# Performance work log

Measured on AMD Instinct MI355X. Metric: run time of the kernel, lower is better.

## Reference

```python
import jax, jax.numpy as jnp
import numpy as np

# Junction tree: C0=(X0,X1f,X2), C1=(X1c,X2,X3f), C2=(X2,X3c,X4)
D0, D1F, D1C, D2, D3F, D3C, D4 = 256, 1024, 256, 256, 512, 256, 512


def _sel(fine: int, coarse: int) -> jnp.ndarray:
    """0/1 selection matrix [fine, coarse]: M[f, f // (fine//coarse)] = 1.
    Equivalent to torch_to_matrix_mul(arange(fine), arange(fine)//r, fine, coarse)."""
    r = fine // coarse
    return (jnp.arange(fine)[:, None] // r == jnp.arange(coarse)[None, :]).astype(jnp.float32)


def setup_inputs() -> dict:
    key = jax.random.key(0)
    k0, k1, k2 = jax.random.split(key, 3)
    theta0 = jax.random.normal(k0, (D0, D1F, D2), dtype=jnp.float32)
    theta1 = jax.random.normal(k1, (D1C, D2, D3F), dtype=jnp.float32)
    theta2 = jax.random.normal(k2, (D2, D3C, D4), dtype=jnp.float32)
    m_x1_fwd = _sel(D1F, D1C)          # (1024, 256): fine X1 -> coarse X1
    m_x1_bwd = m_x1_fwd.T              # (256, 1024): coarse X1 -> fine X1
    m_x3_fwd = _sel(D3F, D3C)          # (512, 256)
    m_x3_bwd = m_x3_fwd.T              # (256, 512)
    return dict(theta0=theta0, theta1=theta1, theta2=theta2,
                m_x1_fwd=m_x1_fwd, m_x1_bwd=m_x1_bwd,
                m_x3_fwd=m_x3_fwd, m_x3_bwd=m_x3_bwd)


def reference(theta0, theta1, theta2, m_x1_fwd, m_x1_bwd, m_x3_fwd, m_x3_bwd):
    # --- forward message C0 -> C1: sum over X0, map X1 fine->coarse, X2 passthrough
    msg01 = jnp.einsum('jc,jf->fc', theta0.sum(axis=0), m_x1_fwd)   # (D1C, D2)
    theta1 = theta1 + msg01[:, :, None]                             # reshape_dims (T,T,F)
    # --- forward message C1 -> C2: sum over X1, X2 passthrough, map X3 fine->coarse
    msg12 = jnp.einsum('cj,jf->cf', theta1.sum(axis=0), m_x3_fwd)   # (D2, D3C)
    theta2 = theta2 + msg12[:, :, None]
    # --- backward message C2 -> C1: sum over X4, subtract stored fwd msg, map X3 coarse->fine
    msg21 = jnp.einsum('cj,jf->cf', theta2.sum(axis=2) - msg12, m_x3_bwd)  # (D2, D3F)
    theta1 = theta1 + msg21[None, :, :]                             # reshape_dims (F,T,T)
    # --- backward message C1 -> C0: sum over X3, subtract stored fwd msg, map X1 coarse->fine
    msg10 = jnp.einsum('jc,jf->fc', theta1.sum(axis=2) - msg01, m_x1_bwd)  # (D1F, D2)
    theta0 = theta0 + msg10[None, :, :]
    return (theta0, theta1, theta2)
```

## Files before the change

### kernel.cpp

```cpp
#include <hip/hip_runtime.h>

#define D0   256
#define D1F  1024
#define D1C  256
#define D2   256
#define D3F  512
#define D3C  256
#define D4   512

#define CB   64
#define NCB  4

#define OFF_MSG01 0
#define OFF_S10   65536
#define OFF_S12   196608
#define OFF_S22   262144
#define OFF_MSG12 327680
#define OFF_S3    393216

typedef float f4 __attribute__((ext_vector_type(4)));

__device__ __forceinline__ float wave_sum(float s) {
#pragma unroll
  for (int off = 32; off; off >>= 1) s += __shfl_down(s, off);
  return s;
}
__device__ __forceinline__ float wave_allsum(float s) {
#pragma unroll
  for (int off = 32; off; off >>= 1) s += __shfl_xor(s, off);
  return s;
}

__global__ __launch_bounds__(256) void k_stage1(const float* __restrict__ t0,
                                                const float* __restrict__ t1,
                                                float* __restrict__ ws, int cb) {
  const int t = threadIdx.x, lane = t & 63, w = t >> 6;
  __shared__ f4 lds[4][2][64];
  if (blockIdx.x < 1024) {
    const int bx = blockIdx.x;
    const int c  = cb * CB + (bx & 63);
    const int ac = bx >> 6;
    float* S10 = ws + OFF_S10;
    float* S12 = ws + OFF_S12;
    f4 accA = {0.f, 0.f, 0.f, 0.f};
    f4 accB = {0.f, 0.f, 0.f, 0.f};
#pragma unroll
    for (int ii = 0; ii < 4; ++ii) {
      const int a = ac * 16 + ii * 4 + w;
      const f4* row = (const f4*)(t1 + ((size_t)a * D2 + c) * D3F);
      f4 v0 = row[lane];
      f4 v1 = row[lane + 64];
      accA += v0; accB += v1;
      float s = v0.x + v0.y + v0.z + v0.w + v1.x + v1.y + v1.z + v1.w;
      s = wave_sum(s);
      if (lane == 0) S12[a * D2 + c] = s;
    }
    lds[w][0][lane] = accA;
    lds[w][1][lane] = accB;
    __syncthreads();
    if (t < 128) {
      const int which = t >> 6, l = t & 63;
      f4 s = lds[0][which][l] + lds[1][which][l] + lds[2][which][l] + lds[3][which][l];
      float* dst = &S10[(size_t)c * D3F + which * 256 + 4 * l];
      atomicAdd(dst + 0, s.x);
      atomicAdd(dst + 1, s.y);
      atomicAdd(dst + 2, s.z);
      atomicAdd(dst + 3, s.w);
    }
  } else {
    const int bx = blockIdx.x - 1024;
    const int f = bx & 255, ic = bx >> 8;
    float* msg01 = ws + OFF_MSG01;
    const int c4 = lane & 15, jr = lane >> 4;
    const int j = 4 * f + jr;
    const f4* t0v = (const f4*)t0;
    f4 acc = {0.f, 0.f, 0.f, 0.f};
#pragma unroll
    for (int ii = 0; ii < 4; ++ii) {
      const int i = ic * 16 + w * 4 + ii;
      acc += t0v[((size_t)i * D1F + j) * 64 + cb * 16 + c4];
    }
#pragma unroll
    for (int off = 32; off >= 16; off >>= 1) {
      acc.x += __shfl_down(acc.x, off);
      acc.y += __shfl_down(acc.y, off);
      acc.z += __shfl_down(acc.z, off);
      acc.w += __shfl_down(acc.w, off);
    }
    if (jr == 0) lds[w][0][c4] = acc;
    __syncthreads();
    if (t < 16) {
      f4 s = lds[0][0][t] + lds[1][0][t] + lds[2][0][t] + lds[3][0][t];
      float* dst = &msg01[f * D2 + cb * CB + 4 * t];
      atomicAdd(dst + 0, s.x);
      atomicAdd(dst + 1, s.y);
      atomicAdd(dst + 2, s.z);
      atomicAdd(dst + 3, s.w);
    }
  }
}

__global__ __launch_bounds__(256) void k_w2mm(const float* __restrict__ t2,
                                              float* __restrict__ out2,
                                              float* __restrict__ ws, int cb) {
  const float* msg01 = ws + OFF_MSG01;
  const float* S10   = ws + OFF_S10;
  float* msg12 = ws + OFF_MSG12;
  float* S22   = ws + OFF_S22;
  const int bx = blockIdx.x;
  const int c = cb * CB + (bx & 63), fc = bx >> 6;
  const int t = threadIdx.x, lane = t & 63, w = t >> 6;
  float p = msg01[lane * D2 + c] + msg01[(lane + 64) * D2 + c]
          + msg01[(lane + 128) * D2 + c] + msg01[(lane + 192) * D2 + c];
  p = wave_allsum(p);
  const float* S10c = S10 + (size_t)c * D3F;
#pragma unroll
  for (int ii = 0; ii < 4; ++ii) {
    const int f = fc * 16 + ii * 4 + w;
    const float m = S10c[2 * f] + S10c[2 * f + 1] + 2.f * p;
    if (lane == 0) msg12[c * D3C + f] = m;
    const size_t base4 = ((size_t)c * D3C + f) * (D4 / 4);
    const f4* row = (const f4*)t2 + base4;
    f4* orow = (f4*)out2 + base4;
    f4 v0 = __builtin_nontemporal_load(row + lane);
    f4 v1 = __builtin_nontemporal_load(row + lane + 64);
    __builtin_nontemporal_store(v0 + m, orow + lane);
    __builtin_nontemporal_store(v1 + m, orow + lane + 64);
    float s = v0.x + v0.y + v0.z + v0.w + v1.x + v1.y + v1.z + v1.w;
    s = wave_sum(s);
    if (lane == 0) S22[c * D3C + f] = s;
  }
}

__global__ __launch_bounds__(256) void k_w1s3(const float* __restrict__ t1,
                                              float* __restrict__ out1,
                                              float* __restrict__ ws, int cb) {
  const float* msg01 = ws + OFF_MSG01;
  const float* S22   = ws + OFF_S22;
  const float* msg12 = ws + OFF_MSG12;
  const int t = threadIdx.x;
  __shared__ float red[4];
  if (blockIdx.x < 8192) {
    const size_t idx = (size_t)blockIdx.x * 256 + t;
    const int k4 = (int)(idx & 127);
    const int cl = (int)((idx >> 7) & 63);
    const int a  = (int)(idx >> 13);
    const int c  = cb * CB + cl;
    const size_t addr = ((size_t)a * D2 + c) * (D3F / 4) + k4;
    f4 v = ((const f4*)t1)[addr];
    const float m = msg01[a * D2 + c];
    const float2 s22v = ((const float2*)S22)[c * 128 + k4];
    const float2 m12v = ((const float2*)msg12)[c * 128 + k4];
    const float s2a = m + s22v.x + 511.f * m12v.x;
    const float s2b = m + s22v.y + 511.f * m12v.y;
    f4 o;
    o.x = v.x + s2a; o.y = v.y + s2a; o.z = v.z + s2b; o.w = v.w + s2b;
    __builtin_nontemporal_store(o, (f4*)out1 + addr);
  } else {
    const float* S12 = ws + OFF_S12;
    float* s3 = ws + OFF_S3;
    const int c = cb * CB + (int)(blockIdx.x - 8192);
    const int lane = t & 63, w = t >> 6;
    const float s2v = S22[c * D3C + t] + 511.f * msg12[c * D3C + t];
    float p = wave_sum(s2v);
    if (lane == 0) red[w] = p;
    __syncthreads();
    const float rs = red[0] + red[1] + red[2] + red[3];
    s3[t * D2 + c] = S12[t * D2 + c] + 511.f * msg01[t * D2 + c] + 2.f * rs;
  }
}

__global__ __launch_bounds__(256) void k_w0(const float* __restrict__ t0,
                                            float* __restrict__ out0,
                                            const float* __restrict__ ws, int cb) {
  const f4* s3v = (const f4*)(ws + OFF_S3);
  const size_t idx = (size_t)blockIdx.x * 256 + threadIdx.x;
  const int c4 = (int)(idx & 15);
  const int j  = (int)((idx >> 4) & 1023);
  const int i  = (int)(idx >> 14);
  const size_t addr = ((size_t)i * D1F + j) * 64 + cb * 16 + c4;
  f4 v = ((const f4*)t0)[addr];
  f4 m = s3v[(j >> 2) * 64 + cb * 16 + c4];
  __builtin_nontemporal_store(v + m, (f4*)out0 + addr);
}

extern "C" void kernel_launch(void* const* d_in, const int* in_sizes, int n_in,
                              void* d_out, int out_size, void* d_ws, size_t ws_size,
                              hipStream_t stream) {
  const float* t0 = (const float*)d_in[0];
  const float* t1 = (const float*)d_in[1];
  const float* t2 = (const float*)d_in[2];
  float* out0 = (float*)d_out;
  float* out1 = out0 + (size_t)D0 * D1F * D2;
  float* out2 = out1 + (size_t)D1C * D2 * D3F;
  float* ws = (float*)d_ws;

  hipMemsetAsync(d_ws, 0, (size_t)OFF_S12 * sizeof(float), stream);

  for (int cb = 0; cb < NCB; ++cb) {
    k_stage1<<<5120, 256, 0, stream>>>(t0, t1, ws, cb);
    k_w2mm<<<1024, 256, 0, stream>>>(t2, out2, ws, cb);
    k_w1s3<<<8256, 256, 0, stream>>>(t1, out1, ws, cb);
    k_w0<<<16384, 256, 0, stream>>>(t0, out0, ws, cb);
  }
}
```

Measured before the change: 958.0 us.

## Drop column chunking and fuse update kernels into single full-width passes

Removes the four-way split over the X2 column dimension, so each stage runs once over the full tensors. The two reductions, the t2 update and a new small s2/s3 kernel each run once. A single merged kernel then writes both the theta1 and theta0 outputs with fully contiguous indexing. The theta0 reduction now reads whole 1KB rows per wave instead of 256B segments and no longer needs the cross-lane shuffle. This cuts launch count from sixteen to four and improves access contiguity. In exchange it gives up the per-chunk working set (about 96MB of t0 and t1) that could stay resident in the last-level cache between the reduce pass and the update pass.

```diff
diff --git a/kernel.cpp b/kernel.cpp
--- a/kernel.cpp
+++ b/kernel.cpp
@@ -8,15 +8,13 @@
 #define D3C  256
 #define D4   512
 
-#define CB   64
-#define NCB  4
-
 #define OFF_MSG01 0
 #define OFF_S10   65536
 #define OFF_S12   196608
 #define OFF_S22   262144
 #define OFF_MSG12 327680
-#define OFF_S3    393216
+#define OFF_S2    393216
+#define OFF_S3    458752
 
 typedef float f4 __attribute__((ext_vector_type(4)));
 
@@ -31,15 +29,15 @@
   return s;
 }
 
-__global__ __launch_bounds__(256) void k_stage1(const float* __restrict__ t0,
+__global__ __launch_bounds__(256) void k_reduce(const float* __restrict__ t0,
                                                 const float* __restrict__ t1,
-                                                float* __restrict__ ws, int cb) {
+                                                float* __restrict__ ws) {
   const int t = threadIdx.x, lane = t & 63, w = t >> 6;
-  __shared__ f4 lds[4][2][64];
-  if (blockIdx.x < 1024) {
+  __shared__ f4 lds[512];
+  if (blockIdx.x < 4096) {
     const int bx = blockIdx.x;
-    const int c  = cb * CB + (bx & 63);
-    const int ac = bx >> 6;
+    const int c  = bx & 255;
+    const int ac = bx >> 8;
     float* S10 = ws + OFF_S10;
     float* S12 = ws + OFF_S12;
     f4 accA = {0.f, 0.f, 0.f, 0.f};
@@ -55,12 +53,13 @@
       s = wave_sum(s);
       if (lane == 0) S12[a * D2 + c] = s;
     }
-    lds[w][0][lane] = accA;
-    lds[w][1][lane] = accB;
+    lds[w * 128 + lane]      = accA;
+    lds[w * 128 + 64 + lane] = accB;
     __syncthreads();
     if (t < 128) {
       const int which = t >> 6, l = t & 63;
-      f4 s = lds[0][which][l] + lds[1][which][l] + lds[2][which][l] + lds[3][which][l];
+      f4 s = lds[which * 64 + l] + lds[128 + which * 64 + l]
+           + lds[256 + which * 64 + l] + lds[384 + which * 64 + l];
       float* dst = &S10[(size_t)c * D3F + which * 256 + 4 * l];
       atomicAdd(dst + 0, s.x);
       atomicAdd(dst + 1, s.y);
@@ -68,30 +67,23 @@
       atomicAdd(dst + 3, s.w);
     }
   } else {
-    const int bx = blockIdx.x - 1024;
+    const int bx = blockIdx.x - 4096;
     const int f = bx & 255, ic = bx >> 8;
     float* msg01 = ws + OFF_MSG01;
-    const int c4 = lane & 15, jr = lane >> 4;
-    const int j = 4 * f + jr;
+    const int c4 = lane;
+    const int j = 4 * f + w;
     const f4* t0v = (const f4*)t0;
     f4 acc = {0.f, 0.f, 0.f, 0.f};
 #pragma unroll
-    for (int ii = 0; ii < 4; ++ii) {
-      const int i = ic * 16 + w * 4 + ii;
-      acc += t0v[((size_t)i * D1F + j) * 64 + cb * 16 + c4];
+    for (int it = 0; it < 16; ++it) {
+      const int i = ic * 16 + it;
+      acc += t0v[((size_t)i * D1F + j) * 64 + c4];
     }
-#pragma unroll
-    for (int off = 32; off >= 16; off >>= 1) {
-      acc.x += __shfl_down(acc.x, off);
-      acc.y += __shfl_down(acc.y, off);
-      acc.z += __shfl_down(acc.z, off);
-      acc.w += __shfl_down(acc.w, off);
-    }
-    if (jr == 0) lds[w][0][c4] = acc;
+    lds[t] = acc;
     __syncthreads();
-    if (t < 16) {
-      f4 s = lds[0][0][t] + lds[1][0][t] + lds[2][0][t] + lds[3][0][t];
-      float* dst = &msg01[f * D2 + cb * CB + 4 * t];
+    if (t < 64) {
+      f4 s = lds[t] + lds[t + 64] + lds[t + 128] + lds[t + 192];
+      float* dst = &msg01[f * D2 + 4 * t];
       atomicAdd(dst + 0, s.x);
       atomicAdd(dst + 1, s.y);
       atomicAdd(dst + 2, s.z);
@@ -102,13 +94,13 @@
 
 __global__ __launch_bounds__(256) void k_w2mm(const float* __restrict__ t2,
                                               float* __restrict__ out2,
-                                              float* __restrict__ ws, int cb) {
+                                              float* __restrict__ ws) {
   const float* msg01 = ws + OFF_MSG01;
   const float* S10   = ws + OFF_S10;
   float* msg12 = ws + OFF_MSG12;
   float* S22   = ws + OFF_S22;
   const int bx = blockIdx.x;
-  const int c = cb * CB + (bx & 63), fc = bx >> 6;
+  const int c = bx & 255, fc = bx >> 8;
   const int t = threadIdx.x, lane = t & 63, w = t >> 6;
   float p = msg01[lane * D2 + c] + msg01[(lane + 64) * D2 + c]
           + msg01[(lane + 128) * D2 + c] + msg01[(lane + 192) * D2 + c];
@@ -132,56 +124,54 @@
   }
 }
 
-__global__ __launch_bounds__(256) void k_w1s3(const float* __restrict__ t1,
-                                              float* __restrict__ out1,
-                                              float* __restrict__ ws, int cb) {
+__global__ __launch_bounds__(256) void k_s2s3(float* __restrict__ ws) {
   const float* msg01 = ws + OFF_MSG01;
+  const float* S12   = ws + OFF_S12;
   const float* S22   = ws + OFF_S22;
   const float* msg12 = ws + OFF_MSG12;
+  float* s2          = ws + OFF_S2;
+  float* s3          = ws + OFF_S3;
+  const int c = blockIdx.x, t = threadIdx.x;
+  const float s2v = S22[c * D3C + t] + 511.f * msg12[c * D3C + t];
+  s2[c * D3C + t] = s2v;
+  float p = wave_sum(s2v);
+  __shared__ float red[4];
+  if ((t & 63) == 0) red[t >> 6] = p;
+  __syncthreads();
+  const float rs = red[0] + red[1] + red[2] + red[3];
+  s3[t * D2 + c] = S12[t * D2 + c] + 511.f * msg01[t * D2 + c] + 2.f * rs;
+}
+
+__global__ __launch_bounds__(256) void k_w1w0(const float* __restrict__ t0,
+                                              const float* __restrict__ t1,
+                                              float* __restrict__ out0,
+                                              float* __restrict__ out1,
+                                              const float* __restrict__ ws) {
   const int t = threadIdx.x;
-  __shared__ float red[4];
-  if (blockIdx.x < 8192) {
+  if (blockIdx.x < 32768) {
+    const float* msg01 = ws + OFF_MSG01;
+    const float* s2    = ws + OFF_S2;
     const size_t idx = (size_t)blockIdx.x * 256 + t;
     const int k4 = (int)(idx & 127);
-    const int cl = (int)((idx >> 7) & 63);
-    const int a  = (int)(idx >> 13);
-    const int c  = cb * CB + cl;
-    const size_t addr = ((size_t)a * D2 + c) * (D3F / 4) + k4;
-    f4 v = ((const f4*)t1)[addr];
+    const int c  = (int)((idx >> 7) & 255);
+    const int a  = (int)(idx >> 15);
+    f4 v = ((const f4*)t1)[idx];
     const float m = msg01[a * D2 + c];
-    const float2 s22v = ((const float2*)S22)[c * 128 + k4];
-    const float2 m12v = ((const float2*)msg12)[c * 128 + k4];
-    const float s2a = m + s22v.x + 511.f * m12v.x;
-    const float s2b = m + s22v.y + 511.f * m12v.y;
+    const float2 s2v = ((const float2*)s2)[c * 128 + k4];
+    const float sa = m + s2v.x;
+    const float sb = m + s2v.y;
     f4 o;
-    o.x = v.x + s2a; o.y = v.y + s2a; o.z = v.z + s2b; o.w = v.w + s2b;
-    __builtin_nontemporal_store(o, (f4*)out1 + addr);
+    o.x = v.x + sa; o.y = v.y + sa; o.z = v.z + sb; o.w = v.w + sb;
+    __builtin_nontemporal_store(o, (f4*)out1 + idx);
   } else {
-    const float* S12 = ws + OFF_S12;
-    float* s3 = ws + OFF_S3;
-    const int c = cb * CB + (int)(blockIdx.x - 8192);
-    const int lane = t & 63, w = t >> 6;
-    const float s2v = S22[c * D3C + t] + 511.f * msg12[c * D3C + t];
-    float p = wave_sum(s2v);
-    if (lane == 0) red[w] = p;
-    __syncthreads();
-    const float rs = red[0] + red[1] + red[2] + red[3];
-    s3[t * D2 + c] = S12[t * D2 + c] + 511.f * msg01[t * D2 + c] + 2.f * rs;
+    const f4* s3v = (const f4*)(ws + OFF_S3);
+    const size_t idx = (size_t)(blockIdx.x - 32768) * 256 + t;
+    const int c4 = (int)(idx & 63);
+    const int j  = (int)((idx >> 6) & 1023);
+    f4 v = ((const f4*)t0)[idx];
+    f4 m = s3v[(j >> 2) * 64 + c4];
+    __builtin_nontemporal_store(v + m, (f4*)out0 + idx);
   }
-}
-
-__global__ __launch_bounds__(256) void k_w0(const float* __restrict__ t0,
-                                            float* __restrict__ out0,
-                                            const float* __restrict__ ws, int cb) {
-  const f4* s3v = (const f4*)(ws + OFF_S3);
-  const size_t idx = (size_t)blockIdx.x * 256 + threadIdx.x;
-  const int c4 = (int)(idx & 15);
-  const int j  = (int)((idx >> 4) & 1023);
-  const int i  = (int)(idx >> 14);
-  const size_t addr = ((size_t)i * D1F + j) * 64 + cb * 16 + c4;
-  f4 v = ((const f4*)t0)[addr];
-  f4 m = s3v[(j >> 2) * 64 + cb * 16 + c4];
-  __builtin_nontemporal_store(v + m, (f4*)out0 + addr);
 }
 
 extern "C" void kernel_launch(void* const* d_in, const int* in_sizes, int n_in,
@@ -197,10 +187,8 @@
 
   hipMemsetAsync(d_ws, 0, (size_t)OFF_S12 * sizeof(float), stream);
 
-  for (int cb = 0; cb < NCB; ++cb) {
-    k_stage1<<<5120, 256, 0, stream>>>(t0, t1, ws, cb);
-    k_w2mm<<<1024, 256, 0, stream>>>(t2, out2, ws, cb);
-    k_w1s3<<<8256, 256, 0, stream>>>(t1, out1, ws, cb);
-    k_w0<<<16384, 256, 0, stream>>>(t0, out0, ws, cb);
-  }
+  k_reduce<<<8192, 256, 0, stream>>>(t0, t1, ws);
+  k_w2mm<<<4096, 256, 0, stream>>>(t2, out2, ws);
+  k_s2s3<<<256, 256, 0, stream>>>(ws);
+  k_w1w0<<<98304, 256, 0, stream>>>(t0, t1, out0, out1, ws);
 }
```

Measured after the change: 925.3 us. 1.04x faster.
